# Kernel tuning notes

Hardware: AMD Instinct MI355X
Metric: run time of the kernel (lower is better)

The kernel has to match this reference:

```python
import jax, jax.numpy as jnp
import numpy as np

BAND = 8          # band_width
DS = 0.1          # diag_subtract
DILATIONS = (1, 2, 4)
EPS_NORM = 1e-6
EPS_GAP = 1e-6
EPS_LN = 1e-5


def _conv1d(x, w, b, dil=1):
    # x: (B, C_in, T), w: (C_out, C_in, K) torch-style OIH
    pad = dil * (w.shape[-1] // 2)  # 'same' padding as in torch module
    y = jax.lax.conv_general_dilated(
        x, w, window_strides=(1,), padding=[(pad, pad)],
        rhs_dilation=(dil,), dimension_numbers=("NCH", "OIH", "NCH"))
    return y + b[None, :, None]


def _strip(feat, mask, w, ds):
    # Banded cosine SSM: strip[b, idx, t] = ((xn[b,t].xn[b,t+|k|]) - ds*[k==0] + 1)/2 * m[t]*m[t+|k|]
    # Mathematically identical to full S = xn xn^T (symmetric) followed by
    # extract_diagonal_strip, but computes only the (2w+1)-wide band.
    xm = feat * mask[:, :, None]
    xn = xm / (jnp.linalg.norm(xm, axis=-1, keepdims=True) + EPS_NORM)
    T = xn.shape[1]
    rows = []
    for k in range(-w, w + 1):
        a = abs(k)
        dot = jnp.einsum("btd,btd->bt", xn[:, :T - a] if a else xn, xn[:, a:])
        s = (dot - (ds if k == 0 else 0.0) + 1.0) * 0.5
        s = s * mask[:, :T - a] * mask[:, a:] if a else s * mask * mask
        rows.append(jnp.pad(s, ((0, 0), (0, a))))
    return jnp.stack(rows, axis=1)  # (B, 2w+1, T)


def _encode(strip, mask, w_in, b_in, stages):
    h = jax.nn.relu(_conv1d(strip, w_in, b_in))
    for (wd, bd, wp, bp, d) in stages:
        h = jax.nn.relu(_conv1d(h, wd, bd, d))   # dilated k=3 conv (dropout=eval no-op)
        h = jax.nn.relu(_conv1d(h, wp, bp))      # pointwise k=1 conv
    m = mask[:, None, :]
    return (h * m).sum(-1) / (m.sum(-1) + EPS_GAP)  # masked GAP -> (B, C)


def setup_inputs() -> dict:
    key = jax.random.key(0)
    ks = jax.random.split(key, 32)
    B, T, D, C, NB = 32, 4096, 256, 64, 2 * BAND + 1
    s = 0.02
    n = lambda k, shp: (jax.random.normal(k, shp, jnp.float32) * s)
    inp = {
        "video_feat": jax.random.normal(ks[0], (B, T, D), jnp.float32),
        "audio_feat": jax.random.normal(ks[1], (B, T, D), jnp.float32),
        "video_mask": jnp.ones((B, T), jnp.float32),
        "audio_mask": jnp.ones((B, T), jnp.float32),
        "w_in": n(ks[2], (C, NB, 1)), "b_in": jnp.zeros((C,), jnp.float32),
        "w_d1": n(ks[3], (C, C, 3)), "b_d1": jnp.zeros((C,), jnp.float32),
        "w_p1": n(ks[4], (C, C, 1)), "b_p1": jnp.zeros((C,), jnp.float32),
        "w_d2": n(ks[5], (C, C, 3)), "b_d2": jnp.zeros((C,), jnp.float32),
        "w_p2": n(ks[6], (C, C, 1)), "b_p2": jnp.zeros((C,), jnp.float32),
        "w_d3": n(ks[7], (C, C, 3)), "b_d3": jnp.zeros((C,), jnp.float32),
        "w_p3": n(ks[8], (C, C, 1)), "b_p3": jnp.zeros((C,), jnp.float32),
        "ln_g": jnp.ones((2 * C,), jnp.float32), "ln_b": jnp.zeros((2 * C,), jnp.float32),
        "mha_w1": n(ks[9], (2 * C, C)), "mha_b1": jnp.zeros((C,), jnp.float32),
        "mha_w2": n(ks[10], (C, 1)), "mha_b2": -jnp.ones((1,), jnp.float32),
        "ffn_w1": n(ks[11], (2 * C, C)), "ffn_b1": jnp.zeros((C,), jnp.float32),
        "ffn_w2": n(ks[12], (C, 1)), "ffn_b2": jnp.zeros((1,), jnp.float32),
    }
    return inp


def reference(video_feat, audio_feat, video_mask, audio_mask,
              w_in, b_in, w_d1, b_d1, w_p1, b_p1, w_d2, b_d2, w_p2, b_p2,
              w_d3, b_d3, w_p3, b_p3, ln_g, ln_b,
              mha_w1, mha_b1, mha_w2, mha_b2, ffn_w1, ffn_b1, ffn_w2, ffn_b2):
    stages = [(w_d1, b_d1, w_p1, b_p1, DILATIONS[0]),
              (w_d2, b_d2, w_p2, b_p2, DILATIONS[1]),
              (w_d3, b_d3, w_p3, b_p3, DILATIONS[2])]
    z_a = _encode(_strip(audio_feat, audio_mask, BAND, DS), audio_mask, w_in, b_in, stages)
    z_v = _encode(_strip(video_feat, video_mask, BAND, DS), video_mask, w_in, b_in, stages)
    f = jnp.concatenate([z_a, z_v], axis=-1)  # (B, 2C), audio first as in torch
    mu = f.mean(-1, keepdims=True)
    var = ((f - mu) ** 2).mean(-1, keepdims=True)
    fn = (f - mu) / jnp.sqrt(var + EPS_LN) * ln_g + ln_b
    g_mha = jax.nn.sigmoid(jax.nn.relu(fn @ mha_w1 + mha_b1) @ mha_w2 + mha_b2)
    g_ffn = jnp.tanh(jax.nn.relu(fn @ ffn_w1 + ffn_b1) @ ffn_w2 + ffn_b2)
    return (g_mha[:, :, None], g_ffn[:, :, None])  # (B,1,1) each
```

## Files before the change

### kernel.cpp

```cpp
#include <hip/hip_runtime.h>
#include <math.h>

#define B_ 32
#define T_ 4096
#define D_ 256
#define C_ 64
#define EPSN 1e-6f
#define EPSG 1e-6f
#define EPSL 1e-5f
#define DS_ 0.1f

typedef short bfrag __attribute__((ext_vector_type(8)));
typedef float f32x4 __attribute__((ext_vector_type(4)));
typedef unsigned short ushort4_t __attribute__((ext_vector_type(4)));
typedef unsigned short ushort8_t __attribute__((ext_vector_type(8)));

static __device__ __forceinline__ unsigned short f2bf(float f) {
    unsigned int u = __builtin_bit_cast(unsigned int, f);
    unsigned int r = u + 0x7fffu + ((u >> 16) & 1u);
    return (unsigned short)(r >> 16);
}
static __device__ __forceinline__ float bf2f(unsigned short u) {
    return __builtin_bit_cast(float, ((unsigned int)u) << 16);
}

static __device__ __forceinline__ f32x4 mfma_bf16(bfrag a, bfrag b, f32x4 c) {
    return __builtin_amdgcn_mfma_f32_16x16x32_bf16(a, b, c, 0, 0, 0);
}

static __device__ __forceinline__ bfrag cvt8(float4 lo, float4 hi) {
    bfrag v;
    v[0] = (short)f2bf(lo.x); v[1] = (short)f2bf(lo.y);
    v[2] = (short)f2bf(lo.z); v[3] = (short)f2bf(lo.w);
    v[4] = (short)f2bf(hi.x); v[5] = (short)f2bf(hi.y);
    v[6] = (short)f2bf(hi.z); v[7] = (short)f2bf(hi.w);
    return v;
}

__global__ __launch_bounds__(256) void prepack_kernel(
    const float* __restrict__ w_in,
    const float* __restrict__ wd0, const float* __restrict__ wp0,
    const float* __restrict__ wd1, const float* __restrict__ wp1,
    const float* __restrict__ wd2, const float* __restrict__ wp2,
    unsigned short* __restrict__ wk)
{
    int idx = blockIdx.x * 256 + threadIdx.x;
    if (idx >= 1024 + 3 * 16384) return;
    if (idx < 1024) {
        int c = idx >> 4, a = idx & 15;
        float wv = 0.f;
        if (a <= 8) {
            wv = w_in[c * 17 + 8 + a];
            if (a > 0) wv += w_in[c * 17 + 8 - a];
        }
        wk[idx] = f2bf(wv);
    } else {
        int i2 = idx - 1024;
        int s = i2 >> 14;
        int r = i2 & 16383;
        const float* wd = s == 0 ? wd0 : (s == 1 ? wd1 : wd2);
        const float* wp = s == 0 ? wp0 : (s == 1 ? wp1 : wp2);
        unsigned short v;
        if (r < 12288) {
            int c = r / 192, k = r - c * 192;
            int tap = k >> 6, ci = k & 63;
            v = f2bf(wd[c * 192 + ci * 3 + tap]);
        } else {
            v = f2bf(wp[r - 12288]);
        }
        wk[idx] = v;
    }
}

#define NT24 43
#define DTP 18

__global__ __launch_bounds__(256, 2) void strip_kernel(
    const float* __restrict__ feat0, const float* __restrict__ mask0,
    const float* __restrict__ feat1, const float* __restrict__ mask1,
    unsigned short* __restrict__ s16g)
{
    __shared__ float dotbuf[4 * 3 * 16 * DTP];
    __shared__ float scl[104];
    __shared__ float msk[104];

    int bid0 = blockIdx.x;
    int bid  = (bid0 & 7) * 344 + (bid0 >> 3);
    int tile = bid % NT24;
    int rem  = bid / NT24;
    int b    = rem & 31;
    int mod  = rem >> 5;
    int mb   = mod * B_ + b;
    const float* feat = mod ? feat1 : feat0;
    const float* mask = mod ? mask1 : mask0;
    int t0 = tile * 96;
    int tid = threadIdx.x;
    int w = tid >> 6, lane = tid & 63;
    int l15 = lane & 15, lg = lane >> 4;

    if (tid < 104) {
        int tg = t0 + tid;
        msk[tid] = (tg < T_) ? mask[(size_t)b * T_ + tg] : 0.f;
    }

    const float* fb = feat + (size_t)b * T_ * D_;

    {
        int i0 = t0 + 24 * w;
        int tA = i0 + l15;      if (tA >= T_) tA = 0;
        int tB = i0 + 16 + l15; if (tB >= T_) tB = 0;
        const float* pA = fb + (size_t)tA * D_ + lg * 8;
        const float* pB = fb + (size_t)tB * D_ + lg * 8;

        float4 fa[16], fbx[16];
        #pragma unroll
        for (int ks = 0; ks < 8; ++ks) {
            fa[2 * ks]      = *(const float4*)(pA + ks * 32);
            fa[2 * ks + 1]  = *(const float4*)(pA + ks * 32 + 4);
            fbx[2 * ks]     = *(const float4*)(pB + ks * 32);
            fbx[2 * ks + 1] = *(const float4*)(pB + ks * 32 + 4);
        }
        __builtin_amdgcn_sched_barrier(0);

        f32x4 a00 = {0.f, 0.f, 0.f, 0.f};
        f32x4 a01 = {0.f, 0.f, 0.f, 0.f};
        f32x4 a11 = {0.f, 0.f, 0.f, 0.f};
        #pragma unroll
        for (int ks = 0; ks < 8; ++ks) {
            bfrag av = cvt8(fa[2 * ks], fa[2 * ks + 1]);
            bfrag bv = cvt8(fbx[2 * ks], fbx[2 * ks + 1]);
            a00 = mfma_bf16(av, av, a00);
            a01 = mfma_bf16(av, bv, a01);
            a11 = mfma_bf16(bv, bv, a11);
        }

        float* base = dotbuf + w * (3 * 16 * DTP);
        #pragma unroll
        for (int r = 0; r < 4; ++r) {
            int row = lg * 4 + r;
            base[row * DTP + l15] = a00[r];
            base[16 * DTP + row * DTP + l15] = a01[r];
            base[32 * DTP + row * DTP + l15] = a11[r];
        }
    }
    __syncthreads();

    if (tid < 104) {
        int ww = tid / 24; if (ww > 3) ww = 3;
        int v = tid - 24 * ww;
        const float* bb = dotbuf + ww * (3 * 16 * DTP);
        float sd = (v < 16) ? bb[v * DTP + v] : bb[32 * DTP + (v - 16) * DTP + (v - 16)];
        float m = msk[tid];
        scl[tid] = m / (m * sqrtf(sd) + EPSN);
    }
    __syncthreads();

    if (tid < 96) {
        int t = t0 + tid;
        if (t < T_) {
            int ww = tid / 24, r = tid - 24 * ww;
            const float* bb = dotbuf + ww * (3 * 16 * DTP);
            float m_t = msk[tid], sc_t = scl[tid];
            ushort8_t o0, o1;
            #pragma unroll
            for (int e = 0; e < 8; ++e) { o0[e] = 0; o1[e] = 0; }
            #pragma unroll
            for (int a = 0; a <= 8; ++a) {
                int c = r + a;
                float dot;
                if (r < 8)       dot = bb[r * DTP + c];
                else if (r < 16) dot = (c < 16) ? bb[r * DTP + c]
                                               : bb[16 * DTP + r * DTP + (c - 16)];
                else             dot = bb[32 * DTP + (r - 16) * DTP + (c - 16)];
                float dn = dot * sc_t * scl[tid + a];
                float s = (dn - (a == 0 ? DS_ : 0.f) + 1.f) * 0.5f * m_t * msk[tid + a];
                if (a < 8) o0[a] = f2bf(s); else o1[0] = f2bf(s);
            }
            unsigned short* dst = s16g + ((size_t)mb * T_ + t) * 16;
            *(ushort8_t*)dst = o0;
            *(ushort8_t*)(dst + 8) = o1;
        }
    }
}

#define TT 128
#define G_ 16
#define WB 160
#define SBP 24
#define OFF_BUFA 8192
#define OFF_BUFB 28672
#define OFF_MLD  49664
#define OFF_RED  50176
#define SMEM_TOT (OFF_RED + 1024)

static __device__ __forceinline__ int swzi(int row, int su, int off) {
    return row * 64 + ((su ^ (row & 7)) << 3) + off;
}

template<int DIL>
static __device__ __forceinline__ void conv_stage(
    const unsigned short* __restrict__ wdg, const unsigned short* __restrict__ wpg,
    unsigned short* __restrict__ bufIn, unsigned short* __restrict__ bufOut,
    const float* __restrict__ b_d, const float* __restrict__ b_p,
    int t0, int l15, int lg, int mt0, int wn)
{
    {
        bfrag ad[2][6];
        float bd[2][4];
        #pragma unroll
        for (int m = 0; m < 2; ++m) {
            int row = (mt0 + m) * 16 + l15;
            #pragma unroll
            for (int ks = 0; ks < 6; ++ks) {
                int tap = ks >> 1, half = ks & 1;
                ad[m][ks] = *(const bfrag*)(wdg + row * 192 + tap * 64 + half * 32 + lg * 8);
            }
            #pragma unroll
            for (int r = 0; r < 4; ++r) bd[m][r] = b_d[(mt0 + m) * 16 + lg * 4 + r];
        }
        for (int nt = wn * 5; nt < wn * 5 + 5; ++nt) {
            int j = nt * 16 + l15;
            f32x4 acc0 = {0.f, 0.f, 0.f, 0.f}, acc1 = {0.f, 0.f, 0.f, 0.f};
            #pragma unroll
            for (int ks = 0; ks < 6; ++ks) {
                int tap = ks >> 1, half = ks & 1;
                int brow = j + (tap - 1) * DIL;
                bfrag bv = *(const bfrag*)(bufIn + swzi(brow, half * 4 + lg, 0));
                acc0 = mfma_bf16(ad[0][ks], bv, acc0);
                acc1 = mfma_bf16(ad[1][ks], bv, acc1);
            }
            int tg = t0 - G_ + j;
            bool valid = (tg >= 0 && tg < T_);
            #pragma unroll
            for (int m = 0; m < 2; ++m) {
                f32x4 acc = m ? acc1 : acc0;
                ushort4_t pk;
                #pragma unroll
                for (int r = 0; r < 4; ++r) {
                    float v = acc[r] + bd[m][r];
                    v = valid ? fmaxf(v, 0.f) : 0.f;
                    pk[r] = f2bf(v);
                }
                *(ushort4_t*)(bufOut + swzi(j, (mt0 + m) * 2 + (lg >> 1), (lg & 1) * 4)) = pk;
            }
        }
    }
    __syncthreads();

    {
        bfrag ap[2][2];
        float bpv[2][4];
        #pragma unroll
        for (int m = 0; m < 2; ++m) {
            int row = (mt0 + m) * 16 + l15;
            #pragma unroll
            for (int half = 0; half < 2; ++half)
                ap[m][half] = *(const bfrag*)(wpg + row * 64 + half * 32 + lg * 8);
            #pragma unroll
            for (int r = 0; r < 4; ++r) bpv[m][r] = b_p[(mt0 + m) * 16 + lg * 4 + r];
        }
        for (int nt = wn * 5; nt < wn * 5 + 5; ++nt) {
            int j = nt * 16 + l15;
            f32x4 acc0 = {0.f, 0.f, 0.f, 0.f}, acc1 = {0.f, 0.f, 0.f, 0.f};
            #pragma unroll
            for (int half = 0; half < 2; ++half) {
                bfrag bv = *(const bfrag*)(bufOut + swzi(j, half * 4 + lg, 0));
                acc0 = mfma_bf16(ap[0][half], bv, acc0);
                acc1 = mfma_bf16(ap[1][half], bv, acc1);
            }
            int tg = t0 - G_ + j;
            bool valid = (tg >= 0 && tg < T_);
            #pragma unroll
            for (int m = 0; m < 2; ++m) {
                f32x4 acc = m ? acc1 : acc0;
                ushort4_t pk;
                #pragma unroll
                for (int r = 0; r < 4; ++r) {
                    float v = acc[r] + bpv[m][r];
                    v = valid ? fmaxf(v, 0.f) : 0.f;
                    pk[r] = f2bf(v);
                }
                *(ushort4_t*)(bufIn + swzi(j, (mt0 + m) * 2 + (lg >> 1), (lg & 1) * 4)) = pk;
            }
        }
    }
    __syncthreads();
}

__global__ __launch_bounds__(256, 3) void conv_mfma_kernel(
    const unsigned short* __restrict__ s16g,
    const float* __restrict__ mask0, const float* __restrict__ mask1,
    const unsigned short* __restrict__ wk,
    const float* __restrict__ b_in,
    const float* __restrict__ b_d1, const float* __restrict__ b_p1,
    const float* __restrict__ b_d2, const float* __restrict__ b_p2,
    const float* __restrict__ b_d3, const float* __restrict__ b_p3,
    float* __restrict__ z_part)
{
    __shared__ __align__(16) char smem[SMEM_TOT];
    unsigned short* sbuf = (unsigned short*)smem;
    unsigned short* bufA = (unsigned short*)(smem + OFF_BUFA);
    unsigned short* bufB = (unsigned short*)(smem + OFF_BUFB);
    float* mld = (float*)(smem + OFF_MLD);
    float* red = (float*)(smem + OFF_RED);

    int bid  = blockIdx.x;
    int tile = bid & 31;
    int b    = (bid >> 5) & 31;
    int mod  = bid >> 10;
    int mb   = mod * B_ + b;
    const float* mask = mod ? mask1 : mask0;
    int t0  = tile * TT;
    int tid = threadIdx.x;
    int lane = tid & 63;
    int w = tid >> 6;
    int l15 = lane & 15, lg = lane >> 4;
    int wm = w >> 1, wn = w & 1;
    int mt0 = wm * 2;

    const unsigned short* weff_g = wk;

    {
        const unsigned short* srow = s16g + (size_t)mb * T_ * 16;
        for (int ch = tid; ch < WB * 2; ch += 256) {
            int j = ch >> 1, q = ch & 1;
            int t = t0 - G_ + j;
            ushort8_t v = {0, 0, 0, 0, 0, 0, 0, 0};
            if (t >= 0 && t < T_) v = *(const ushort8_t*)(srow + (size_t)t * 16 + q * 8);
            *(ushort8_t*)(sbuf + j * SBP + q * 8) = v;
        }
        if (tid < TT) {
            int tg = t0 + tid;
            mld[tid] = (tg < T_) ? mask[(size_t)b * T_ + tg] : 0.f;
        }
    }
    __syncthreads();

    {
        int lg2 = lg & 1;
        bfrag a_in[2];
        float bi[2][4];
        #pragma unroll
        for (int m = 0; m < 2; ++m) {
            int row = (mt0 + m) * 16 + l15;
            a_in[m] = *(const bfrag*)(weff_g + row * 16 + lg2 * 8);
            #pragma unroll
            for (int r = 0; r < 4; ++r) bi[m][r] = b_in[(mt0 + m) * 16 + lg * 4 + r];
        }
        for (int nt = wn * 5; nt < wn * 5 + 5; ++nt) {
            int j = nt * 16 + l15;
            bfrag bv = {0, 0, 0, 0, 0, 0, 0, 0};
            if (lg < 2) bv = *(const bfrag*)(sbuf + j * SBP + lg * 8);
            f32x4 acc0 = {0.f, 0.f, 0.f, 0.f}, acc1 = {0.f, 0.f, 0.f, 0.f};
            acc0 = mfma_bf16(a_in[0], bv, acc0);
            acc1 = mfma_bf16(a_in[1], bv, acc1);
            int tg = t0 - G_ + j;
            bool valid = (tg >= 0 && tg < T_);
            #pragma unroll
            for (int m = 0; m < 2; ++m) {
                f32x4 acc = m ? acc1 : acc0;
                ushort4_t pk;
                #pragma unroll
                for (int r = 0; r < 4; ++r) {
                    float v = acc[r] + bi[m][r];
                    v = valid ? fmaxf(v, 0.f) : 0.f;
                    pk[r] = f2bf(v);
                }
                *(ushort4_t*)(bufA + swzi(j, (mt0 + m) * 2 + (lg >> 1), (lg & 1) * 4)) = pk;
            }
        }
    }
    __syncthreads();

    conv_stage<1>(wk + 1024,             wk + 1024 + 12288,             bufA, bufB, b_d1, b_p1, t0, l15, lg, mt0, wn);
    conv_stage<2>(wk + 1024 + 16384,     wk + 1024 + 16384 + 12288,     bufA, bufB, b_d2, b_p2, t0, l15, lg, mt0, wn);
    conv_stage<4>(wk + 1024 + 2 * 16384, wk + 1024 + 2 * 16384 + 12288, bufA, bufB, b_d3, b_p3, t0, l15, lg, mt0, wn);

    {
        int c = tid & 63, g = tid >> 6;
        float acc = 0.f;
        #pragma unroll 4
        for (int i = 0; i < 32; ++i) {
            int jj = g * 32 + i;
            int r = G_ + jj;
            acc += bf2f(bufA[swzi(r, c >> 3, c & 7)]) * mld[jj];
        }
        red[g * 64 + c] = acc;
    }
    __syncthreads();
    if (tid < 64) {
        float z = red[tid] + red[64 + tid] + red[128 + tid] + red[192 + tid];
        z_part[((size_t)mb * 32 + tile) * 64 + tid] = z;
    }
}

__global__ __launch_bounds__(128) void gates_kernel(
    const float* __restrict__ z_part,
    const float* __restrict__ mask0, const float* __restrict__ mask1,
    const float* __restrict__ ln_g, const float* __restrict__ ln_b,
    const float* __restrict__ mha_w1, const float* __restrict__ mha_b1,
    const float* __restrict__ mha_w2, const float* __restrict__ mha_b2,
    const float* __restrict__ ffn_w1, const float* __restrict__ ffn_b1,
    const float* __restrict__ ffn_w2, const float* __restrict__ ffn_b2,
    float* __restrict__ out)
{
    __shared__ float fn[128];
    __shared__ float red[4];
    __shared__ float msum[2];
    int b = blockIdx.x, tid = threadIdx.x;
    int mod = tid >> 6, c = tid & 63;

    float z = 0.f;
    for (int tl = 0; tl < 32; ++tl)
        z += z_part[((size_t)(mod * B_ + b) * 32 + tl) * 64 + c];

    const float* mk = mod ? mask1 : mask0;
    float ms = 0.f;
    for (int t = c; t < T_; t += 64) ms += mk[(size_t)b * T_ + t];
    #pragma unroll
    for (int o = 32; o > 0; o >>= 1) ms += __shfl_xor(ms, o);
    if (c == 0) msum[mod] = ms;
    __syncthreads();

    float fv = z / (msum[mod] + EPSG);
    float s1 = fv, s2 = fv * fv;
    #pragma unroll
    for (int o = 32; o > 0; o >>= 1) { s1 += __shfl_xor(s1, o); s2 += __shfl_xor(s2, o); }
    if (c == 0) { red[mod * 2] = s1; red[mod * 2 + 1] = s2; }
    __syncthreads();

    float mu  = (red[0] + red[2]) * (1.0f / 128.0f);
    float ex2 = (red[1] + red[3]) * (1.0f / 128.0f);
    float var = ex2 - mu * mu;
    float fnv = (fv - mu) * rsqrtf(var + EPSL) * ln_g[tid] + ln_b[tid];
    fn[tid] = fnv;
    __syncthreads();

    const float* W1 = mod ? ffn_w1 : mha_w1;
    const float* B1 = mod ? ffn_b1 : mha_b1;
    const float* W2 = mod ? ffn_w2 : mha_w2;
    const float* B2 = mod ? ffn_b2 : mha_b2;
    float r = B1[c];
    for (int i = 0; i < 128; ++i) r += fn[i] * W1[i * 64 + c];
    r = fmaxf(r, 0.f);
    float g = r * W2[c];
    #pragma unroll
    for (int o = 32; o > 0; o >>= 1) g += __shfl_xor(g, o);
    if (c == 0) {
        g += B2[0];
        out[mod * B_ + b] = mod ? tanhf(g) : 1.0f / (1.0f + expf(-g));
    }
}

extern "C" void kernel_launch(void* const* d_in, const int* in_sizes, int n_in,
                              void* d_out, int out_size, void* d_ws, size_t ws_size,
                              hipStream_t stream) {
    const float* video_feat = (const float*)d_in[0];
    const float* audio_feat = (const float*)d_in[1];
    const float* video_mask = (const float*)d_in[2];
    const float* audio_mask = (const float*)d_in[3];
    const float* w_in = (const float*)d_in[4];
    const float* b_in = (const float*)d_in[5];
    const float* w_d1 = (const float*)d_in[6];
    const float* b_d1 = (const float*)d_in[7];
    const float* w_p1 = (const float*)d_in[8];
    const float* b_p1 = (const float*)d_in[9];
    const float* w_d2 = (const float*)d_in[10];
    const float* b_d2 = (const float*)d_in[11];
    const float* w_p2 = (const float*)d_in[12];
    const float* b_p2 = (const float*)d_in[13];
    const float* w_d3 = (const float*)d_in[14];
    const float* b_d3 = (const float*)d_in[15];
    const float* w_p3 = (const float*)d_in[16];
    const float* b_p3 = (const float*)d_in[17];
    const float* ln_g = (const float*)d_in[18];
    const float* ln_b = (const float*)d_in[19];
    const float* mha_w1 = (const float*)d_in[20];
    const float* mha_b1 = (const float*)d_in[21];
    const float* mha_w2 = (const float*)d_in[22];
    const float* mha_b2 = (const float*)d_in[23];
    const float* ffn_w1 = (const float*)d_in[24];
    const float* ffn_b1 = (const float*)d_in[25];
    const float* ffn_w2 = (const float*)d_in[26];
    const float* ffn_b2 = (const float*)d_in[27];

    unsigned short* s16g = (unsigned short*)d_ws;
    float* z_part = (float*)((char*)d_ws + (size_t)2 * B_ * T_ * 16 * 2);
    unsigned short* wk = (unsigned short*)((char*)z_part + (size_t)2 * B_ * 32 * 64 * 4);

    prepack_kernel<<<dim3(196), dim3(256), 0, stream>>>(
        w_in, w_d1, w_p1, w_d2, w_p2, w_d3, w_p3, wk);

    strip_kernel<<<dim3(2 * B_ * NT24), dim3(256), 0, stream>>>(
        audio_feat, audio_mask, video_feat, video_mask, s16g);

    conv_mfma_kernel<<<dim3(2 * B_ * (T_ / TT)), dim3(256), 0, stream>>>(
        s16g, audio_mask, video_mask, wk, b_in,
        b_d1, b_p1, b_d2, b_p2, b_d3, b_p3, z_part);

    gates_kernel<<<dim3(B_), dim3(128), 0, stream>>>(
        z_part, audio_mask, video_mask, ln_g, ln_b,
        mha_w1, mha_b1, mha_w2, mha_b2, ffn_w1, ffn_b1, ffn_w2, ffn_b2,
        (float*)d_out);
}
```

Before: 145.5 us.

## Stage strip features into LDS via async global_load_lds in two halves

The strip kernel now loads each 104-row feature tile into a swizzled LDS buffer with direct global-to-LDS loads, split into two D-halves. It waits on the first half with a partial vmcnt wait and starts the MFMA dot products while the second half is still arriving. The aim is to cut register pressure from holding 32 float4s per thread and to overlap loading with compute. In exchange it uses about 121KB of dynamic LDS per block, which limits occupancy to one block per CU, and it drops the 2-blocks launch bound.

```diff
diff --git a/kernel.cpp b/kernel.cpp
--- a/kernel.cpp
+++ b/kernel.cpp
@@ -35,6 +35,12 @@
     v[4] = (short)f2bf(hi.x); v[5] = (short)f2bf(hi.y);
     v[6] = (short)f2bf(hi.z); v[7] = (short)f2bf(hi.w);
     return v;
+}
+
+static __device__ __forceinline__ void gload_lds16(const float* g, float* l) {
+    __builtin_amdgcn_global_load_lds(
+        (const __attribute__((address_space(1))) unsigned int*)(g),
+        (__attribute__((address_space(3))) unsigned int*)(l), 16, 0, 0);
 }
 
 __global__ __launch_bounds__(256) void prepack_kernel(
@@ -73,16 +79,19 @@
 }
 
 #define NT24 43
-#define DTP 18
-
-__global__ __launch_bounds__(256, 2) void strip_kernel(
+#define XHALF 13312
+#define SMEM_STRIP (30288 * 4)
+
+__global__ __launch_bounds__(256) void strip_kernel(
     const float* __restrict__ feat0, const float* __restrict__ mask0,
     const float* __restrict__ feat1, const float* __restrict__ mask1,
     unsigned short* __restrict__ s16g)
 {
-    __shared__ float dotbuf[4 * 3 * 16 * DTP];
-    __shared__ float scl[104];
-    __shared__ float msk[104];
+    extern __shared__ float sm[];
+    float* xbuf   = sm;
+    float* dotbuf = sm + 26624;
+    float* scl    = sm + 30080;
+    float* msk    = sm + 30184;
 
     int bid0 = blockIdx.x;
     int bid  = (bid0 & 7) * 344 + (bid0 >> 3);
@@ -98,58 +107,79 @@
     int w = tid >> 6, lane = tid & 63;
     int l15 = lane & 15, lg = lane >> 4;
 
+    const float* fb = feat + (size_t)b * T_ * D_;
+
+    auto stage_half = [&](int h, float* buf) {
+        #pragma unroll
+        for (int i = 0; i < 13; ++i) {
+            int gi = w * 13 + i;
+            int row = gi * 2 + (lane >> 5);
+            int tg = t0 + row; if (tg >= T_) tg = T_ - 1;
+            const float* gp = fb + (size_t)tg * D_ + h * 128
+                              + (((lane & 31) ^ (row & 7)) << 2);
+            gload_lds16(gp, buf + gi * 256);
+        }
+    };
+
+    int rA = 24 * w + l15;
+    int rB = rA + 16;
+    int a7 = rA & 7, b7 = rB & 7;
+    f32x4 a00 = {0.f, 0.f, 0.f, 0.f};
+    f32x4 a01 = {0.f, 0.f, 0.f, 0.f};
+    f32x4 a11 = {0.f, 0.f, 0.f, 0.f};
+
+    auto compute_half = [&](const float* xb) {
+        const float* pa = xb + rA * 128;
+        const float* pb = xb + rB * 128;
+        #pragma unroll
+        for (int ks = 0; ks < 4; ++ks) {
+            int s0 = ks * 8 + lg * 2;
+            float4 a0 = *(const float4*)(pa + ((s0 ^ a7) << 2));
+            float4 a1 = *(const float4*)(pa + (((s0 + 1) ^ a7) << 2));
+            float4 b0 = *(const float4*)(pb + ((s0 ^ b7) << 2));
+            float4 b1 = *(const float4*)(pb + (((s0 + 1) ^ b7) << 2));
+            bfrag av = cvt8(a0, a1);
+            bfrag bv = cvt8(b0, b1);
+            a00 = mfma_bf16(av, av, a00);
+            a01 = mfma_bf16(av, bv, a01);
+            a11 = mfma_bf16(bv, bv, a11);
+        }
+    };
+
+    stage_half(0, xbuf);
+    stage_half(1, xbuf + XHALF);
+
+    asm volatile("s_waitcnt vmcnt(13)" ::: "memory");
+    __builtin_amdgcn_sched_barrier(0);
+    __builtin_amdgcn_s_barrier();
+    compute_half(xbuf);
+
+    asm volatile("s_waitcnt vmcnt(0)" ::: "memory");
+    __builtin_amdgcn_sched_barrier(0);
+    __builtin_amdgcn_s_barrier();
+    compute_half(xbuf + XHALF);
+
+    {
+        float* base = dotbuf + w * 864;
+        #pragma unroll
+        for (int r = 0; r < 4; ++r) {
+            int row = lg * 4 + r;
+            base[row * 18 + l15] = a00[r];
+            base[288 + row * 18 + l15] = a01[r];
+            base[576 + row * 18 + l15] = a11[r];
+        }
+    }
     if (tid < 104) {
         int tg = t0 + tid;
         msk[tid] = (tg < T_) ? mask[(size_t)b * T_ + tg] : 0.f;
     }
-
-    const float* fb = feat + (size_t)b * T_ * D_;
-
-    {
-        int i0 = t0 + 24 * w;
-        int tA = i0 + l15;      if (tA >= T_) tA = 0;
-        int tB = i0 + 16 + l15; if (tB >= T_) tB = 0;
-        const float* pA = fb + (size_t)tA * D_ + lg * 8;
-        const float* pB = fb + (size_t)tB * D_ + lg * 8;
-
-        float4 fa[16], fbx[16];
-        #pragma unroll
-        for (int ks = 0; ks < 8; ++ks) {
-            fa[2 * ks]      = *(const float4*)(pA + ks * 32);
-            fa[2 * ks + 1]  = *(const float4*)(pA + ks * 32 + 4);
-            fbx[2 * ks]     = *(const float4*)(pB + ks * 32);
-            fbx[2 * ks + 1] = *(const float4*)(pB + ks * 32 + 4);
-        }
-        __builtin_amdgcn_sched_barrier(0);
-
-        f32x4 a00 = {0.f, 0.f, 0.f, 0.f};
-        f32x4 a01 = {0.f, 0.f, 0.f, 0.f};
-        f32x4 a11 = {0.f, 0.f, 0.f, 0.f};
-        #pragma unroll
-        for (int ks = 0; ks < 8; ++ks) {
-            bfrag av = cvt8(fa[2 * ks], fa[2 * ks + 1]);
-            bfrag bv = cvt8(fbx[2 * ks], fbx[2 * ks + 1]);
-            a00 = mfma_bf16(av, av, a00);
-            a01 = mfma_bf16(av, bv, a01);
-            a11 = mfma_bf16(bv, bv, a11);
-        }
-
-        float* base = dotbuf + w * (3 * 16 * DTP);
-        #pragma unroll
-        for (int r = 0; r < 4; ++r) {
-            int row = lg * 4 + r;
-            base[row * DTP + l15] = a00[r];
-            base[16 * DTP + row * DTP + l15] = a01[r];
-            base[32 * DTP + row * DTP + l15] = a11[r];
-        }
-    }
     __syncthreads();
 
     if (tid < 104) {
         int ww = tid / 24; if (ww > 3) ww = 3;
         int v = tid - 24 * ww;
-        const float* bb = dotbuf + ww * (3 * 16 * DTP);
-        float sd = (v < 16) ? bb[v * DTP + v] : bb[32 * DTP + (v - 16) * DTP + (v - 16)];
+        const float* bb = dotbuf + ww * 864;
+        float sd = (v < 16) ? bb[v * 18 + v] : bb[576 + (v - 16) * 18 + (v - 16)];
         float m = msk[tid];
         scl[tid] = m / (m * sqrtf(sd) + EPSN);
     }
@@ -159,7 +189,7 @@
         int t = t0 + tid;
         if (t < T_) {
             int ww = tid / 24, r = tid - 24 * ww;
-            const float* bb = dotbuf + ww * (3 * 16 * DTP);
+            const float* bb = dotbuf + ww * 864;
             float m_t = msk[tid], sc_t = scl[tid];
             ushort8_t o0, o1;
             #pragma unroll
@@ -168,10 +198,10 @@
             for (int a = 0; a <= 8; ++a) {
                 int c = r + a;
                 float dot;
-                if (r < 8)       dot = bb[r * DTP + c];
-                else if (r < 16) dot = (c < 16) ? bb[r * DTP + c]
-                                               : bb[16 * DTP + r * DTP + (c - 16)];
-                else             dot = bb[32 * DTP + (r - 16) * DTP + (c - 16)];
+                if (r < 8)       dot = bb[r * 18 + c];
+                else if (r < 16) dot = (c < 16) ? bb[r * 18 + c]
+                                               : bb[288 + r * 18 + (c - 16)];
+                else             dot = bb[576 + (r - 16) * 18 + (c - 16)];
                 float dn = dot * sc_t * scl[tid + a];
                 float s = (dn - (a == 0 ? DS_ : 0.f) + 1.f) * 0.5f * m_t * msk[tid + a];
                 if (a < 8) o0[a] = f2bf(s); else o1[0] = f2bf(s);
@@ -491,7 +521,9 @@
     prepack_kernel<<<dim3(196), dim3(256), 0, stream>>>(
         w_in, w_d1, w_p1, w_d2, w_p2, w_d3, w_p3, wk);
 
-    strip_kernel<<<dim3(2 * B_ * NT24), dim3(256), 0, stream>>>(
+    hipFuncSetAttribute((const void*)strip_kernel,
+                        hipFuncAttributeMaxDynamicSharedMemorySize, SMEM_STRIP);
+    strip_kernel<<<dim3(2 * B_ * NT24), dim3(256), SMEM_STRIP, stream>>>(
         audio_feat, audio_mask, video_feat, video_mask, s16g);
 
     conv_mfma_kernel<<<dim3(2 * B_ * (T_ / TT)), dim3(256), 0, stream>>>(
```

New measurement: 162.6 us. 1.12x slower.
